# Performance work log

Hardware: AMD Instinct MI355X
Metric: run time of the kernel (lower is better)

## Reference

```python
import jax, jax.numpy as jnp
import numpy as np

N = 50000
E = 800000
D = 128
H = 8
DH = D // H


def setup_inputs() -> dict:
    key = jax.random.key(0)
    ks = jax.random.split(key, 8)
    x = jax.random.normal(ks[0], (N, D), dtype=jnp.float32)
    src = jax.random.randint(ks[1], (E,), 0, N, dtype=jnp.int32)
    dst = jax.random.randint(ks[2], (E,), 0, N, dtype=jnp.int32)
    s = 1.0 / np.sqrt(D)
    w_qkv = jax.random.uniform(ks[3], (3 * D, D), jnp.float32, -s, s)
    b_qkv = jax.random.uniform(ks[4], (3 * D,), jnp.float32, -s, s)
    w_out = jax.random.uniform(ks[5], (D, D), jnp.float32, -s, s)
    b_out = jax.random.uniform(ks[6], (D,), jnp.float32, -s, s)
    return {"x": x, "src": src, "dst": dst, "w_qkv": w_qkv, "b_qkv": b_qkv,
            "w_out": w_out, "b_out": b_out}


def reference(x, src, dst, w_qkv, b_qkv, w_out, b_out):
    n = x.shape[0]
    coef = 1.0 / np.sqrt(DH)
    qkv = (x @ w_qkv.T + b_qkv).reshape(n, H, 3 * DH)
    q, k, v = qkv[..., :DH], qkv[..., DH:2 * DH], qkv[..., 2 * DH:]
    # per-edge scores: dot(k[src], q[dst]) per head -> [E, H]
    scores = jnp.einsum('ehd,ehd->eh', k[src], q[dst]) * coef
    # edge softmax over edges sharing the same destination node
    smax = jax.ops.segment_max(scores, dst, num_segments=n)  # [N, H]
    smax = jnp.where(jnp.isfinite(smax), smax, 0.0)
    ex = jnp.exp(scores - smax[dst])                          # [E, H]
    denom = jax.ops.segment_sum(ex, dst, num_segments=n)      # [N, H]
    probs = ex / jnp.maximum(denom[dst], 1e-30)
    # weighted aggregation of source values -> [N, H, DH]
    agg = jax.ops.segment_sum(probs[:, :, None] * v[src], dst, num_segments=n)
    out = agg.reshape(n, D) @ w_out.T + b_out
    return out
```

## Files before the change

### kernel.cpp

```cpp
#include <hip/hip_runtime.h>
#include <math.h>

#define DD   128
#define NQKV 384
#define CAP  128

typedef __attribute__((ext_vector_type(8))) short          bf16x8;
typedef __attribute__((ext_vector_type(8))) unsigned short ushort8;
typedef __attribute__((ext_vector_type(4))) float          f32x4;

__device__ __forceinline__ unsigned short f2bf(float f) {
    unsigned u = __float_as_uint(f);
    u += 0x7fffu + ((u >> 16) & 1u);
    return (unsigned short)(u >> 16);
}
__device__ __forceinline__ float bf2f(unsigned short h) {
    return __uint_as_float(((unsigned)h) << 16);
}
__device__ __forceinline__ float bflo(unsigned u) { return __uint_as_float(u << 16); }
__device__ __forceinline__ float bfhi(unsigned u) { return __uint_as_float(u & 0xffff0000u); }

#define NWQ8 (NQKV * DD / 8)
#define NWO8 (DD * DD / 8)

__global__ void prep_kernel(const float* __restrict__ w_qkv, const float* __restrict__ w_out,
                            unsigned short* __restrict__ wq_hi, unsigned short* __restrict__ wq_lo,
                            unsigned short* __restrict__ wo_hi, unsigned short* __restrict__ wo_lo,
                            int* __restrict__ counts, int nzc4) {
    int i = blockIdx.x * blockDim.x + threadIdx.x;
    if (i < nzc4) {
        ((int4*)counts)[i] = make_int4(0, 0, 0, 0);
        return;
    }
    int j = i - nzc4;
    const float* srcp;
    unsigned short *hip_, *lop_;
    if (j < NWQ8)            { srcp = w_qkv + (size_t)j * 8;          hip_ = wq_hi + (size_t)j * 8;          lop_ = wq_lo + (size_t)j * 8; }
    else if (j < NWQ8+NWO8)  { int k = j - NWQ8; srcp = w_out + (size_t)k * 8; hip_ = wo_hi + (size_t)k * 8; lop_ = wo_lo + (size_t)k * 8; }
    else return;
    const float4* p = (const float4*)srcp;
    float4 a = p[0], b = p[1];
    float v[8] = {a.x, a.y, a.z, a.w, b.x, b.y, b.z, b.w};
    ushort8 vh, vl;
    #pragma unroll
    for (int t = 0; t < 8; ++t) {
        unsigned short h = f2bf(v[t]);
        vh[t] = h;
        vl[t] = f2bf(v[t] - bf2f(h));
    }
    *(ushort8*)hip_ = vh;
    *(ushort8*)lop_ = vl;
}

__global__ void scatter_fixed_kernel(const int* __restrict__ src, const int* __restrict__ dst,
                                     int* __restrict__ counts, int* __restrict__ lists, int E) {
    int t = blockIdx.x * blockDim.x + threadIdx.x;
    int base = t * 8;
    if (base >= E) return;
    if (base + 8 <= E) {
        int4 d0 = *(const int4*)(dst + base);
        int4 d1 = *(const int4*)(dst + base + 4);
        int4 s0 = *(const int4*)(src + base);
        int4 s1 = *(const int4*)(src + base + 4);
        int dd[8] = {d0.x, d0.y, d0.z, d0.w, d1.x, d1.y, d1.z, d1.w};
        int ss[8] = {s0.x, s0.y, s0.z, s0.w, s1.x, s1.y, s1.z, s1.w};
        int pos[8];
        #pragma unroll
        for (int i = 0; i < 8; ++i) pos[i] = atomicAdd(&counts[dd[i]], 1);
        #pragma unroll
        for (int i = 0; i < 8; ++i)
            if (pos[i] < CAP) lists[(size_t)dd[i] * CAP + pos[i]] = ss[i];
    } else {
        for (int e = base; e < E; ++e) {
            int d = dst[e];
            int pos = atomicAdd(&counts[d], 1);
            if (pos < CAP) lists[(size_t)d * CAP + pos] = src[e];
        }
    }
}

#define TM 128
#define TN 128
#define LDA 40

__global__ __launch_bounds__(256, 3) void qkv_gemm_kernel(
    const float* __restrict__ X,
    const unsigned short* __restrict__ Bh, const unsigned short* __restrict__ Bl,
    const float* __restrict__ bias, float* __restrict__ Cq,
    unsigned short* __restrict__ Ck, unsigned short* __restrict__ Cv, int M)
{
    __shared__ unsigned short As[TM * LDA];
    __shared__ unsigned short Bs_h[TN * LDA];
    __shared__ unsigned short Bs_l[TN * LDA];

    const int tid  = threadIdx.x;
    const int l    = tid & 63;
    const int wv   = tid >> 6;
    const int quad = l >> 4;
    const int l15  = l & 15;
    const int wm   = (wv & 1) * 64;
    const int wn   = (wv >> 1) * 64;
    const int m0   = blockIdx.x * TM;
    const int n0   = blockIdx.y * TN;

    f32x4 acc[4][4];
    #pragma unroll
    for (int i = 0; i < 4; ++i)
        #pragma unroll
        for (int j = 0; j < 4; ++j) acc[i][j] = (f32x4)0.f;

    #pragma unroll
    for (int kc = 0; kc < DD; kc += 32) {
        #pragma unroll
        for (int it = 0; it < 2; ++it) {
            int idx = tid + it * 256;
            int row = idx >> 2;
            int pc  = idx & 3;
            int loff = row * LDA + pc * 8;
            ushort8 va = 0;
            if (m0 + row < M) {
                const float4* xp = (const float4*)(X + (size_t)(m0 + row) * DD + kc + pc * 8);
                float4 a0 = xp[0], a1 = xp[1];
                float v[8] = {a0.x,a0.y,a0.z,a0.w,a1.x,a1.y,a1.z,a1.w};
                #pragma unroll
                for (int t = 0; t < 8; ++t) va[t] = f2bf(v[t]);
            }
            *(ushort8*)&As[loff] = va;
            size_t gb = (size_t)(n0 + row) * DD + kc + pc * 8;
            *(ushort8*)&Bs_h[loff] = *(const ushort8*)(Bh + gb);
            *(ushort8*)&Bs_l[loff] = *(const ushort8*)(Bl + gb);
        }
        __syncthreads();

        bf16x8 ah[4], bh[4], bl[4];
        #pragma unroll
        for (int mt = 0; mt < 4; ++mt)
            ah[mt] = *(const bf16x8*)&As[(wm + mt * 16 + l15) * LDA + quad * 8];
        #pragma unroll
        for (int nt = 0; nt < 4; ++nt) {
            int off = (wn + nt * 16 + l15) * LDA + quad * 8;
            bh[nt] = *(const bf16x8*)&Bs_h[off];
            bl[nt] = *(const bf16x8*)&Bs_l[off];
        }
        #pragma unroll
        for (int mt = 0; mt < 4; ++mt)
            #pragma unroll
            for (int nt = 0; nt < 4; ++nt) {
                acc[mt][nt] = __builtin_amdgcn_mfma_f32_16x16x32_bf16(ah[mt], bh[nt], acc[mt][nt], 0, 0, 0);
                acc[mt][nt] = __builtin_amdgcn_mfma_f32_16x16x32_bf16(ah[mt], bl[nt], acc[mt][nt], 0, 0, 0);
            }
        __syncthreads();
    }

    #pragma unroll
    for (int nt = 0; nt < 4; ++nt) {
        int j = n0 + wn + nt * 16 + l15;
        float bj = bias[j];
        int h = j / 48;
        int r = j - h * 48;
        int seg = (r >= 32) ? 2 : ((r >= 16) ? 1 : 0);
        int bc  = h * 16 + r - seg * 16;
        #pragma unroll
        for (int mt = 0; mt < 4; ++mt)
            #pragma unroll
            for (int rr = 0; rr < 4; ++rr) {
                int m = m0 + wm + mt * 16 + quad * 4 + rr;
                if (m >= M) continue;
                float val = acc[mt][nt][rr] + bj;
                if (seg == 0)      Cq[(size_t)m * DD + bc] = val;
                else if (seg == 1) Ck[(size_t)m * DD + bc] = f2bf(val);
                else               Cv[(size_t)m * DD + bc] = f2bf(val);
            }
    }
}

__global__ __launch_bounds__(256, 3) void out_gemm_kernel(
    const unsigned short* __restrict__ A,
    const unsigned short* __restrict__ Bh, const unsigned short* __restrict__ Bl,
    const float* __restrict__ bias, float* __restrict__ C, int M)
{
    __shared__ unsigned short As[TM * LDA];
    __shared__ unsigned short Bs_h[TN * LDA];
    __shared__ unsigned short Bs_l[TN * LDA];

    const int tid  = threadIdx.x;
    const int l    = tid & 63;
    const int wv   = tid >> 6;
    const int quad = l >> 4;
    const int l15  = l & 15;
    const int wm   = (wv & 1) * 64;
    const int wn   = (wv >> 1) * 64;
    const int m0   = blockIdx.x * TM;

    f32x4 acc[4][4];
    #pragma unroll
    for (int i = 0; i < 4; ++i)
        #pragma unroll
        for (int j = 0; j < 4; ++j) acc[i][j] = (f32x4)0.f;

    #pragma unroll
    for (int kc = 0; kc < DD; kc += 32) {
        #pragma unroll
        for (int it = 0; it < 2; ++it) {
            int idx = tid + it * 256;
            int row = idx >> 2;
            int pc  = idx & 3;
            int loff = row * LDA + pc * 8;
            ushort8 va = 0;
            if (m0 + row < M)
                va = *(const ushort8*)(A + (size_t)(m0 + row) * DD + kc + pc * 8);
            *(ushort8*)&As[loff] = va;
            size_t gb = (size_t)row * DD + kc + pc * 8;
            *(ushort8*)&Bs_h[loff] = *(const ushort8*)(Bh + gb);
            *(ushort8*)&Bs_l[loff] = *(const ushort8*)(Bl + gb);
        }
        __syncthreads();

        bf16x8 ah[4], bh[4], bl[4];
        #pragma unroll
        for (int mt = 0; mt < 4; ++mt)
            ah[mt] = *(const bf16x8*)&As[(wm + mt * 16 + l15) * LDA + quad * 8];
        #pragma unroll
        for (int nt = 0; nt < 4; ++nt) {
            int off = (wn + nt * 16 + l15) * LDA + quad * 8;
            bh[nt] = *(const bf16x8*)&Bs_h[off];
            bl[nt] = *(const bf16x8*)&Bs_l[off];
        }
        #pragma unroll
        for (int mt = 0; mt < 4; ++mt)
            #pragma unroll
            for (int nt = 0; nt < 4; ++nt) {
                acc[mt][nt] = __builtin_amdgcn_mfma_f32_16x16x32_bf16(ah[mt], bh[nt], acc[mt][nt], 0, 0, 0);
                acc[mt][nt] = __builtin_amdgcn_mfma_f32_16x16x32_bf16(ah[mt], bl[nt], acc[mt][nt], 0, 0, 0);
            }
        __syncthreads();
    }

    #pragma unroll
    for (int nt = 0; nt < 4; ++nt) {
        int j = wn + nt * 16 + l15;
        float bj = bias[j];
        #pragma unroll
        for (int mt = 0; mt < 4; ++mt)
            #pragma unroll
            for (int rr = 0; rr < 4; ++rr) {
                int m = m0 + wm + mt * 16 + quad * 4 + rr;
                if (m < M) C[(size_t)m * DD + j] = acc[mt][nt][rr] + bj;
            }
    }
}

__global__ __launch_bounds__(256) void wave_attn_kernel(
    const float* __restrict__ q, const unsigned short* __restrict__ kbf,
    const unsigned short* __restrict__ vbf, const int* __restrict__ lists,
    const int* __restrict__ counts,
    unsigned short* __restrict__ agg, int N)
{
    const int lane = threadIdx.x & 63;
    const int n = blockIdx.x * 4 + (threadIdx.x >> 6);
    if (n >= N) return;

    const int h = lane >> 3;
    const int e = lane & 7;

    const int deg = min(counts[n], CAP);
    const size_t obase = (size_t)n * DD + 2 * lane;
    if (deg == 0) {
        *(unsigned*)(agg + obase) = 0u;
        return;
    }

    const int row0 = n * CAP;
    const float4* qp = (const float4*)(q + (size_t)n * DD + h * 16);
    const float4 q0 = qp[0], q1 = qp[1], q2 = qp[2], q3 = qp[3];

    float l_run = 0.f;
    float acc0 = 0.f, acc1 = 0.f;

    int cur = lists[row0 + min(e, deg - 1)];

    for (int c = 0; c < deg; c += 8) {
        const int cnt = min(8, deg - c);

        const int nxt = lists[row0 + min(c + 8 + e, deg - 1)];
        const uint4* kp = (const uint4*)(kbf + (size_t)cur * DD + h * 16);
        const uint4 ka = kp[0], kb = kp[1];

        unsigned vv[8];
        #pragma unroll
        for (int ee = 0; ee < 8; ++ee) {
            const int sv = __shfl(cur, ee);
            vv[ee] = *(const unsigned*)(vbf + (size_t)sv * DD + 2 * lane);
        }

        float s = bflo(ka.x)*q0.x + bfhi(ka.x)*q0.y + bflo(ka.y)*q0.z + bfhi(ka.y)*q0.w
                + bflo(ka.z)*q1.x + bfhi(ka.z)*q1.y + bflo(ka.w)*q1.z + bfhi(ka.w)*q1.w
                + bflo(kb.x)*q2.x + bfhi(kb.x)*q2.y + bflo(kb.y)*q2.z + bfhi(kb.y)*q2.w
                + bflo(kb.z)*q3.x + bfhi(kb.z)*q3.y + bflo(kb.w)*q3.z + bfhi(kb.w)*q3.w;

        const float p = (e < cnt) ? __expf(s * 0.25f) : 0.f;
        l_run += p;

        #pragma unroll
        for (int ee = 0; ee < 8; ++ee) {
            const float pe = __shfl(p, (lane & 0x38) | ee);
            acc0 = fmaf(pe, bflo(vv[ee]), acc0);
            acc1 = fmaf(pe, bfhi(vv[ee]), acc1);
        }

        cur = nxt;
    }

    l_run += __shfl_xor(l_run, 1);
    l_run += __shfl_xor(l_run, 2);
    l_run += __shfl_xor(l_run, 4);

    const float inv = 1.f / fmaxf(l_run, 1e-30f);
    const float o0 = acc0 * inv, o1 = acc1 * inv;
    *(unsigned*)(agg + obase) = (unsigned)f2bf(o0) | ((unsigned)f2bf(o1) << 16);
}

extern "C" void kernel_launch(void* const* d_in, const int* in_sizes, int n_in,
                              void* d_out, int out_size, void* d_ws, size_t ws_size,
                              hipStream_t stream) {
    const float* x     = (const float*)d_in[0];
    const int*   src   = (const int*)  d_in[1];
    const int*   dst   = (const int*)  d_in[2];
    const float* w_qkv = (const float*)d_in[3];
    const float* b_qkv = (const float*)d_in[4];
    const float* w_out = (const float*)d_in[5];
    const float* b_out = (const float*)d_in[6];
    float* out = (float*)d_out;

    const int N = in_sizes[0] / DD;
    const int E = in_sizes[1];

    typedef unsigned short u16;
    char* ws = (char*)d_ws;
    float* qf  = (float*)ws; ws += (size_t)N * DD * sizeof(float);
    u16* kbf   = (u16*)ws;   ws += (size_t)N * DD * sizeof(u16);
    u16* vbf   = (u16*)ws;   ws += (size_t)N * DD * sizeof(u16);
    u16* aggb  = (u16*)ws;   ws += (size_t)N * DD * sizeof(u16);
    u16* wq_hi = (u16*)ws;   ws += (size_t)NQKV * DD * sizeof(u16);
    u16* wq_lo = (u16*)ws;   ws += (size_t)NQKV * DD * sizeof(u16);
    u16* wo_hi = (u16*)ws;   ws += (size_t)DD * DD * sizeof(u16);
    u16* wo_lo = (u16*)ws;   ws += (size_t)DD * DD * sizeof(u16);
    int* counts = (int*)ws;  ws += (size_t)((N + 3) / 4 * 4) * sizeof(int);
    int* lists  = (int*)ws;  ws += (size_t)N * CAP * sizeof(int);

    const int nzc4 = (N + 3) / 4;
    const int npb  = (nzc4 + NWQ8 + NWO8 + 255) / 256;
    const int nsb  = ((E + 7) / 8 + 255) / 256;
    const int MB   = (N + TM - 1) / TM;

    prep_kernel<<<npb, 256, 0, stream>>>(w_qkv, w_out, wq_hi, wq_lo, wo_hi, wo_lo,
                                         counts, nzc4);
    scatter_fixed_kernel<<<nsb, 256, 0, stream>>>(src, dst, counts, lists, E);

    qkv_gemm_kernel<<<dim3(MB, NQKV / TN), 256, 0, stream>>>(
        x, wq_hi, wq_lo, b_qkv, qf, kbf, vbf, N);

    wave_attn_kernel<<<(N + 3) / 4, 256, 0, stream>>>(
        qf, kbf, vbf, lists, counts, aggb, N);

    out_gemm_kernel<<<MB, 256, 0, stream>>>(
        aggb, wo_hi, wo_lo, b_out, out, N);
}
```

Before: 235.8 us.

## Store Q in bf16, reorder QKV grid, and prefetch next edge chunk in attention

Q is now written as bf16 rather than fp32, which halves its store in the QKV GEMM and its load in the attention kernel. The QKV GEMM grid is transposed so the three column blocks of one row tile run next to each other, letting them share the X tile in cache. The attention kernel software-pipelines the K and V gathers, loading the next 8-edge chunk while computing the current one. The costs are more registers in the attention loop and lower precision for Q.

```diff
diff --git a/kernel.cpp b/kernel.cpp
--- a/kernel.cpp
+++ b/kernel.cpp
@@ -86,7 +86,7 @@
 __global__ __launch_bounds__(256, 3) void qkv_gemm_kernel(
     const float* __restrict__ X,
     const unsigned short* __restrict__ Bh, const unsigned short* __restrict__ Bl,
-    const float* __restrict__ bias, float* __restrict__ Cq,
+    const float* __restrict__ bias, unsigned short* __restrict__ Cq,
     unsigned short* __restrict__ Ck, unsigned short* __restrict__ Cv, int M)
 {
     __shared__ unsigned short As[TM * LDA];
@@ -100,8 +100,8 @@
     const int l15  = l & 15;
     const int wm   = (wv & 1) * 64;
     const int wn   = (wv >> 1) * 64;
-    const int m0   = blockIdx.x * TM;
-    const int n0   = blockIdx.y * TN;
+    const int n0   = blockIdx.x * TN;
+    const int m0   = blockIdx.y * TM;
 
     f32x4 acc[4][4];
     #pragma unroll
@@ -160,16 +160,13 @@
         int r = j - h * 48;
         int seg = (r >= 32) ? 2 : ((r >= 16) ? 1 : 0);
         int bc  = h * 16 + r - seg * 16;
+        unsigned short* dstp = (seg == 0 ? Cq : (seg == 1 ? Ck : Cv));
         #pragma unroll
         for (int mt = 0; mt < 4; ++mt)
             #pragma unroll
             for (int rr = 0; rr < 4; ++rr) {
                 int m = m0 + wm + mt * 16 + quad * 4 + rr;
-                if (m >= M) continue;
-                float val = acc[mt][nt][rr] + bj;
-                if (seg == 0)      Cq[(size_t)m * DD + bc] = val;
-                else if (seg == 1) Ck[(size_t)m * DD + bc] = f2bf(val);
-                else               Cv[(size_t)m * DD + bc] = f2bf(val);
+                if (m < M) dstp[(size_t)m * DD + bc] = f2bf(acc[mt][nt][rr] + bj);
             }
     }
 }
@@ -251,7 +248,7 @@
 }
 
 __global__ __launch_bounds__(256) void wave_attn_kernel(
-    const float* __restrict__ q, const unsigned short* __restrict__ kbf,
+    const unsigned short* __restrict__ qbf, const unsigned short* __restrict__ kbf,
     const unsigned short* __restrict__ vbf, const int* __restrict__ lists,
     const int* __restrict__ counts,
     unsigned short* __restrict__ agg, int N)
@@ -271,26 +268,43 @@
     }
 
     const int row0 = n * CAP;
-    const float4* qp = (const float4*)(q + (size_t)n * DD + h * 16);
-    const float4 q0 = qp[0], q1 = qp[1], q2 = qp[2], q3 = qp[3];
+
+    const uint4* qp = (const uint4*)(qbf + (size_t)n * DD + h * 16);
+    const uint4 qa = qp[0], qb = qp[1];
+    const float4 q0 = make_float4(bflo(qa.x), bfhi(qa.x), bflo(qa.y), bfhi(qa.y));
+    const float4 q1 = make_float4(bflo(qa.z), bfhi(qa.z), bflo(qa.w), bfhi(qa.w));
+    const float4 q2 = make_float4(bflo(qb.x), bfhi(qb.x), bflo(qb.y), bfhi(qb.y));
+    const float4 q3 = make_float4(bflo(qb.z), bfhi(qb.z), bflo(qb.w), bfhi(qb.w));
+
+    int cur = lists[row0 + min(e, deg - 1)];
+    int nxt = lists[row0 + min(8 + e, deg - 1)];
+
+    const uint4* kp0 = (const uint4*)(kbf + (size_t)cur * DD + h * 16);
+    uint4 ka = kp0[0], kb = kp0[1];
+    unsigned vv[8];
+    #pragma unroll
+    for (int ee = 0; ee < 8; ++ee)
+        vv[ee] = *(const unsigned*)(vbf + (size_t)__shfl(cur, ee) * DD + 2 * lane);
 
     float l_run = 0.f;
     float acc0 = 0.f, acc1 = 0.f;
 
-    int cur = lists[row0 + min(e, deg - 1)];
-
     for (int c = 0; c < deg; c += 8) {
         const int cnt = min(8, deg - c);
-
-        const int nxt = lists[row0 + min(c + 8 + e, deg - 1)];
-        const uint4* kp = (const uint4*)(kbf + (size_t)cur * DD + h * 16);
-        const uint4 ka = kp[0], kb = kp[1];
-
-        unsigned vv[8];
-        #pragma unroll
-        for (int ee = 0; ee < 8; ++ee) {
-            const int sv = __shfl(cur, ee);
-            vv[ee] = *(const unsigned*)(vbf + (size_t)sv * DD + 2 * lane);
+        const bool more = (c + 8 < deg);
+
+        const int nn = lists[row0 + min(c + 16 + e, deg - 1)];
+
+        uint4 k1a = ka, k1b = kb;
+        unsigned vn[8];
+        #pragma unroll
+        for (int ee = 0; ee < 8; ++ee) vn[ee] = vv[ee];
+        if (more) {
+            const uint4* kp = (const uint4*)(kbf + (size_t)nxt * DD + h * 16);
+            k1a = kp[0]; k1b = kp[1];
+            #pragma unroll
+            for (int ee = 0; ee < 8; ++ee)
+                vn[ee] = *(const unsigned*)(vbf + (size_t)__shfl(nxt, ee) * DD + 2 * lane);
         }
 
         float s = bflo(ka.x)*q0.x + bfhi(ka.x)*q0.y + bflo(ka.y)*q0.z + bfhi(ka.y)*q0.w
@@ -308,7 +322,10 @@
             acc1 = fmaf(pe, bfhi(vv[ee]), acc1);
         }
 
-        cur = nxt;
+        ka = k1a; kb = k1b;
+        #pragma unroll
+        for (int ee = 0; ee < 8; ++ee) vv[ee] = vn[ee];
+        cur = nxt; nxt = nn;
     }
 
     l_run += __shfl_xor(l_run, 1);
@@ -337,7 +354,7 @@
 
     typedef unsigned short u16;
     char* ws = (char*)d_ws;
-    float* qf  = (float*)ws; ws += (size_t)N * DD * sizeof(float);
+    u16* qbf   = (u16*)ws;   ws += (size_t)N * DD * sizeof(u16);
     u16* kbf   = (u16*)ws;   ws += (size_t)N * DD * sizeof(u16);
     u16* vbf   = (u16*)ws;   ws += (size_t)N * DD * sizeof(u16);
     u16* aggb  = (u16*)ws;   ws += (size_t)N * DD * sizeof(u16);
@@ -357,11 +374,11 @@
                                          counts, nzc4);
     scatter_fixed_kernel<<<nsb, 256, 0, stream>>>(src, dst, counts, lists, E);
 
-    qkv_gemm_kernel<<<dim3(MB, NQKV / TN), 256, 0, stream>>>(
-        x, wq_hi, wq_lo, b_qkv, qf, kbf, vbf, N);
+    qkv_gemm_kernel<<<dim3(NQKV / TN, MB), 256, 0, stream>>>(
+        x, wq_hi, wq_lo, b_qkv, qbf, kbf, vbf, N);
 
     wave_attn_kernel<<<(N + 3) / 4, 256, 0, stream>>>(
-        qf, kbf, vbf, lists, counts, aggb, N);
+        qbf, kbf, vbf, lists, counts, aggb, N);
 
     out_gemm_kernel<<<MB, 256, 0, stream>>>(
         aggb, wo_hi, wo_lo, b_out, out, N);
```

Result: no change. 235.4 us (-0.2%).
